# Optimization experiments

Hardware: AMD Instinct MI355X
Metric: run time of the kernel (lower is better)

Reference implementation:

```python
import jax, jax.numpy as jnp
import numpy as np

D_MODEL = 1024
NUM_HEADS = 16
HEAD_DIM = D_MODEL // NUM_HEADS


def setup_inputs() -> dict:
    key = jax.random.key(0)
    ks = jax.random.split(key, 11)
    B, N = 2, 2048
    s = 1.0 / np.sqrt(D_MODEL)
    return {
        "query": jax.random.normal(ks[0], (B, N, D_MODEL), jnp.float32),
        "key":   jax.random.normal(ks[1], (B, N, D_MODEL), jnp.float32),
        "value": jax.random.normal(ks[2], (B, N, D_MODEL), jnp.float32),
        "Wq": jax.random.normal(ks[3], (D_MODEL, D_MODEL), jnp.float32) * s,
        "bq": jax.random.normal(ks[4], (D_MODEL,), jnp.float32) * 0.01,
        "Wk": jax.random.normal(ks[5], (D_MODEL, D_MODEL), jnp.float32) * s,
        "bk": jax.random.normal(ks[6], (D_MODEL,), jnp.float32) * 0.01,
        "Wv": jax.random.normal(ks[7], (D_MODEL, D_MODEL), jnp.float32) * s,
        "bv": jax.random.normal(ks[8], (D_MODEL,), jnp.float32) * 0.01,
        "Wo": jax.random.normal(ks[9], (D_MODEL, D_MODEL), jnp.float32) * s,
        "bo": jax.random.normal(ks[10], (D_MODEL,), jnp.float32) * 0.01,
    }


def _split_heads(x):
    # [B, N, d_model] -> [B, H, N, head_dim]
    B, N, _ = x.shape
    return x.reshape(B, N, NUM_HEADS, HEAD_DIM).transpose(0, 2, 1, 3)


def reference(query, key, value, Wq, bq, Wk, bk, Wv, bv, Wo, bo):
    B, N, _ = query.shape
    q = _split_heads(query @ Wq.T + bq)  # [B,H,N,dh]
    k = _split_heads(key @ Wk.T + bk)
    v = _split_heads(value @ Wv.T + bv)
    # NOTE: faithful to source: no 1/sqrt(head_dim) scaling.
    scores = jnp.einsum("bhnd,bhmd->bhnm", q, k)
    attn = jax.nn.softmax(scores, axis=-1)
    out = jnp.einsum("bhnm,bhmd->bhnd", attn, v)
    out = out.transpose(0, 2, 1, 3).reshape(B, N, D_MODEL)
    return out @ Wo.T + bo
```

## Files before the change

### kernel.cpp

```cpp
#include <hip/hip_runtime.h>
#include <cstdint>

#define DEV __device__ __forceinline__

typedef __bf16 bf16x8 __attribute__((ext_vector_type(8)));
typedef short s16x8 __attribute__((ext_vector_type(8)));
typedef float f32x4 __attribute__((ext_vector_type(4)));
typedef unsigned short u16;

constexpr int D_MODEL = 1024;
constexpr int SEQ = 2048;
constexpr float LOG2E = 1.4426950408889634f;
constexpr float SHIFT = 64.0f;

DEV u16 f2bf(float f) {
  uint32_t u = __float_as_uint(f);
  u += 0x7fff + ((u >> 16) & 1);
  return (u16)(u >> 16);
}

DEV void load_lds16(const void* g, void* l) {
  __builtin_amdgcn_global_load_lds((const __attribute__((address_space(1))) void*)g,
                                   (__attribute__((address_space(3))) void*)l, 16, 0, 0);
}

struct ConvArgs {
  const float* src[7];
  u16* dst[7];
};

__global__ __launch_bounds__(256) void convert_kernel(ConvArgs a) {
  const int bid = blockIdx.x;
  int t, base;
  if (bid < 12288) { t = bid >> 12; base = (bid & 4095) << 10; }
  else { int r = bid - 12288; t = 3 + (r >> 10); base = (r & 1023) << 10; }
  const int i = base + threadIdx.x * 4;
  const float4 v = *(const float4*)(a.src[t] + i);
  ushort4 o;
  o.x = f2bf(v.x); o.y = f2bf(v.y); o.z = f2bf(v.z); o.w = f2bf(v.w);
  *(ushort4*)(a.dst[t] + i) = o;
}

struct GemmArgs {
  const u16* A[3];
  const u16* W[3];
  const float* bias[3];
  u16* out[3];
  float scale[3];
};

__global__ __launch_bounds__(256, 2) void gemm_qkv(GemmArgs args) {
  __shared__ u16 lds[2][2][128 * 64];
  const int bid = blockIdx.x;
  const int xcd = bid & 7, j = bid >> 3;
  const int z = j >> 5;
  const int r0 = j & 31;
  const int m0 = (xcd * 4 + (r0 >> 3)) * 128;
  const int n0 = (r0 & 7) * 128;
  const u16* __restrict__ A = args.A[z];
  const u16* __restrict__ W = args.W[z];
  const int tid = threadIdx.x;
  const int lane = tid & 63, wid = tid >> 6;
  const int quad = lane >> 4, l16 = lane & 15;
  const int wm = wid >> 1, wn = wid & 1;

  f32x4 acc[4][4] = {};

#define GSTAGE(T, B)                                                              \
  {                                                                               \
    _Pragma("unroll")                                                             \
    for (int p = 0; p < 4; ++p) {                                                 \
      int c = p * 256 + tid;                                                      \
      int row = c >> 3;                                                           \
      int g = ((c & 7) ^ (row & 7)) * 8;                                          \
      load_lds16(A + (size_t)(m0 + row) * D_MODEL + (T) * 64 + g, &lds[B][0][c * 8]); \
      load_lds16(W + (size_t)(n0 + row) * D_MODEL + (T) * 64 + g, &lds[B][1][c * 8]); \
    }                                                                             \
  }

  GSTAGE(0, 0);
  __syncthreads();

  for (int kt = 0; kt < 16; ++kt) {
    if (kt + 1 < 16) GSTAGE(kt + 1, (kt + 1) & 1);
    const u16* lA = lds[kt & 1][0];
    const u16* lB = lds[kt & 1][1];
#pragma unroll
    for (int ks = 0; ks < 2; ++ks) {
      bf16x8 af[4], bfr[4];
#pragma unroll
      for (int mt = 0; mt < 4; ++mt) {
        int r = wm * 64 + mt * 16 + l16;
        int ch = (ks * 4 + quad) ^ (r & 7);
        af[mt] = *(const bf16x8*)&lA[r * 64 + ch * 8];
      }
#pragma unroll
      for (int nt = 0; nt < 4; ++nt) {
        int r = wn * 64 + nt * 16 + l16;
        int ch = (ks * 4 + quad) ^ (r & 7);
        bfr[nt] = *(const bf16x8*)&lB[r * 64 + ch * 8];
      }
#pragma unroll
      for (int mt = 0; mt < 4; ++mt)
#pragma unroll
        for (int nt = 0; nt < 4; ++nt)
          acc[mt][nt] = __builtin_amdgcn_mfma_f32_16x16x32_bf16(af[mt], bfr[nt], acc[mt][nt], 0, 0, 0);
    }
    __syncthreads();
  }
#undef GSTAGE

  const float* __restrict__ bias = args.bias[z];
  u16* out = args.out[z];
  float sc = args.scale[z];
  if (z == 2) {
#pragma unroll
    for (int nt = 0; nt < 4; ++nt) {
      int col = n0 + wn * 64 + nt * 16 + l16;
      float bv = bias[col];
      int h = col >> 6, d = col & 63;
#pragma unroll
      for (int mt = 0; mt < 4; ++mt) {
        int mb = m0 + wm * 64 + mt * 16 + quad * 4;
        int b = mb >> 11, tt = mb & 2047;
        ushort4 o;
        o.x = f2bf(acc[mt][nt][0] + bv);
        o.y = f2bf(acc[mt][nt][1] + bv);
        o.z = f2bf(acc[mt][nt][2] + bv);
        o.w = f2bf(acc[mt][nt][3] + bv);
        *(ushort4*)(out + ((size_t)(b * 16 + h) * 64 + d) * SEQ + tt) = o;
      }
    }
  } else {
#pragma unroll
    for (int nt = 0; nt < 4; ++nt) {
      int col = n0 + wn * 64 + nt * 16 + l16;
      float bv = bias[col];
      int h = col >> 6, d = col & 63;
#pragma unroll
      for (int mt = 0; mt < 4; ++mt) {
        int mb = m0 + wm * 64 + mt * 16 + quad * 4;
#pragma unroll
        for (int r = 0; r < 4; ++r) {
          int tok = mb + r;
          int b = tok >> 11, tt = tok & 2047;
          out[(((size_t)(b * 16 + h) * SEQ + tt) << 6) + d] = f2bf((acc[mt][nt][r] + bv) * sc);
        }
      }
    }
  }
}

__global__ __launch_bounds__(256, 2) void gemm_out(const u16* __restrict__ A,
                                                   const u16* __restrict__ W,
                                                   const float* __restrict__ bias,
                                                   float* __restrict__ out) {
  __shared__ u16 lds[2][(128 + 64) * 64];
  const int bid = blockIdx.x;
  const int xcd = bid & 7, j = bid >> 3;
  const int m0 = (xcd * 4 + (j >> 4)) * 128;
  const int n0 = (j & 15) * 64;
  const int tid = threadIdx.x;
  const int lane = tid & 63, wid = tid >> 6;
  const int quad = lane >> 4, l16 = lane & 15;
  const int wm = wid >> 1, wn = wid & 1;

  f32x4 acc[4][2] = {};

#define OSTAGE(T, B)                                                              \
  {                                                                               \
    _Pragma("unroll")                                                             \
    for (int p = 0; p < 4; ++p) {                                                 \
      int c = p * 256 + tid;                                                      \
      int row = c >> 3;                                                           \
      int g = ((c & 7) ^ (row & 7)) * 8;                                          \
      load_lds16(A + (size_t)(m0 + row) * D_MODEL + (T) * 64 + g, &lds[B][c * 8]); \
    }                                                                             \
    _Pragma("unroll")                                                             \
    for (int p = 0; p < 2; ++p) {                                                 \
      int c = p * 256 + tid;                                                      \
      int row = c >> 3;                                                           \
      int g = ((c & 7) ^ (row & 7)) * 8;                                          \
      load_lds16(W + (size_t)(n0 + row) * D_MODEL + (T) * 64 + g,                 \
                 &lds[B][128 * 64 + c * 8]);                                      \
    }                                                                             \
  }

  OSTAGE(0, 0);
  __syncthreads();

  for (int kt = 0; kt < 16; ++kt) {
    if (kt + 1 < 16) OSTAGE(kt + 1, (kt + 1) & 1);
    const u16* lA = lds[kt & 1];
    const u16* lW = lds[kt & 1] + 128 * 64;
#pragma unroll
    for (int ks = 0; ks < 2; ++ks) {
      bf16x8 af[4], wf[2];
#pragma unroll
      for (int mt = 0; mt < 4; ++mt) {
        int r = wm * 64 + mt * 16 + l16;
        int ch = (ks * 4 + quad) ^ (r & 7);
        af[mt] = *(const bf16x8*)&lA[r * 64 + ch * 8];
      }
#pragma unroll
      for (int nt = 0; nt < 2; ++nt) {
        int r = wn * 32 + nt * 16 + l16;
        int ch = (ks * 4 + quad) ^ (r & 7);
        wf[nt] = *(const bf16x8*)&lW[r * 64 + ch * 8];
      }
#pragma unroll
      for (int mt = 0; mt < 4; ++mt)
#pragma unroll
        for (int nt = 0; nt < 2; ++nt)
          acc[mt][nt] = __builtin_amdgcn_mfma_f32_16x16x32_bf16(af[mt], wf[nt], acc[mt][nt], 0, 0, 0);
    }
    __syncthreads();
  }
#undef OSTAGE

#pragma unroll
  for (int nt = 0; nt < 2; ++nt) {
    int col = n0 + wn * 32 + nt * 16 + l16;
    float bv = bias[col];
#pragma unroll
    for (int mt = 0; mt < 4; ++mt) {
      int mb = m0 + wm * 64 + mt * 16 + quad * 4;
#pragma unroll
      for (int r = 0; r < 4; ++r)
        out[(size_t)(mb + r) * D_MODEL + col] = acc[mt][nt][r] + bv;
    }
  }
}

__global__ __launch_bounds__(512, 4) void attn_kernel(const u16* __restrict__ Q,
                                                      const u16* __restrict__ K,
                                                      const u16* __restrict__ Vt,
                                                      u16* __restrict__ O) {
  __shared__ u16 sm[4][2][64 * 64];
  const int bid = blockIdx.x;
  const int xcd = bid & 7, jj = bid >> 3;
  const int bh = xcd + 8 * (jj >> 4);
  const int q0 = (jj & 15) * 128;
  const int tid = threadIdx.x;
  const int lane = tid & 63, w = tid >> 6;
  const int quad = lane >> 4, l16 = lane & 15;
  const int kb = w & 1;
  const int pair = w >> 1;

  const u16* kbase = K + (size_t)bh * SEQ * 64;
  const u16* vtbase = Vt + (size_t)bh * 64 * SEQ;

  bf16x8 qf[2][2];
#pragma unroll
  for (int qh = 0; qh < 2; ++qh) {
    const u16* qrow = Q + ((size_t)bh * SEQ + q0 + pair * 32 + qh * 16 + l16) * 64;
    qf[qh][0] = *(const bf16x8*)(qrow + quad * 8);
    qf[qh][1] = *(const bf16x8*)(qrow + 32 + quad * 8);
  }

  bf16x8 onesA;
  {
    __bf16 v = (l16 == 0) ? (__bf16)1.0f : (__bf16)0.0f;
#pragma unroll
    for (int j = 0; j < 8; ++j) onesA[j] = v;
  }

  f32x4 acc[2][5] = {};
  const f32x4 minit = {-SHIFT, -SHIFT, -SHIFT, -SHIFT};

#define STAGE(T, B)                                                               \
  {                                                                               \
    int c = tid;                                                                  \
    int row = c >> 3;                                                             \
    int km = (row & 32) | (((row >> 2) & 3) << 3) | (((row >> 4) & 1) << 2) |     \
             (row & 3);                                                           \
    int g = ((c & 7) ^ (row & 7)) * 8;                                            \
    load_lds16(kbase + (size_t)((T) * 64 + km) * 64 + g, &sm[B][0][c * 8]);       \
    load_lds16(vtbase + (size_t)row * SEQ + (T) * 64 + g, &sm[B][1][c * 8]);      \
  }

  STAGE(0, 0);
  STAGE(1, 1);
  STAGE(2, 2);
  asm volatile("s_waitcnt vmcnt(4)" ::: "memory");
  __builtin_amdgcn_s_barrier();
  __builtin_amdgcn_sched_barrier(0);

  for (int t = 0; t < SEQ / 64; ++t) {
    if (t + 3 < SEQ / 64) STAGE(t + 3, (t + 3) & 3);
    const u16* lK = sm[t & 3][0];
    const u16* lV = sm[t & 3][1];

    bf16x8 kf[2][2];
#pragma unroll
    for (int nt = 0; nt < 2; ++nt) {
      int r = kb * 32 + nt * 16 + l16;
#pragma unroll
      for (int ks = 0; ks < 2; ++ks) {
        int ch = (ks * 4 + quad) ^ (r & 7);
        kf[nt][ks] = *(const bf16x8*)&lK[r * 64 + ch * 8];
      }
    }

    f32x4 s[2][2];
    __builtin_amdgcn_s_setprio(1);
#pragma unroll
    for (int qh = 0; qh < 2; ++qh) {
      s[qh][0] = __builtin_amdgcn_mfma_f32_16x16x32_bf16(kf[0][0], qf[qh][0], minit, 0, 0, 0);
      s[qh][0] = __builtin_amdgcn_mfma_f32_16x16x32_bf16(kf[0][1], qf[qh][1], s[qh][0], 0, 0, 0);
      s[qh][1] = __builtin_amdgcn_mfma_f32_16x16x32_bf16(kf[1][0], qf[qh][0], minit, 0, 0, 0);
      s[qh][1] = __builtin_amdgcn_mfma_f32_16x16x32_bf16(kf[1][1], qf[qh][1], s[qh][1], 0, 0, 0);
    }
    __builtin_amdgcn_s_setprio(0);

    s16x8 pf[2];
#pragma unroll
    for (int qh = 0; qh < 2; ++qh) {
      bf16x8 pb;
#pragma unroll
      for (int r = 0; r < 4; ++r) {
        pb[r] = (__bf16)__builtin_amdgcn_exp2f(s[qh][0][r]);
        pb[4 + r] = (__bf16)__builtin_amdgcn_exp2f(s[qh][1][r]);
      }
      pf[qh] = __builtin_bit_cast(s16x8, pb);
    }

    bf16x8 vf[4];
#pragma unroll
    for (int dt = 0; dt < 4; ++dt) {
      int row = dt * 16 + l16;
      int ch = (kb * 4 + quad) ^ (row & 7);
      vf[dt] = *(const bf16x8*)&lV[row * 64 + ch * 8];
    }
    __builtin_amdgcn_s_setprio(1);
#pragma unroll
    for (int dt = 0; dt < 4; ++dt)
#pragma unroll
      for (int qh = 0; qh < 2; ++qh)
        acc[qh][dt] = __builtin_amdgcn_mfma_f32_16x16x32_bf16(
            vf[dt], __builtin_bit_cast(bf16x8, pf[qh]), acc[qh][dt], 0, 0, 0);
#pragma unroll
    for (int qh = 0; qh < 2; ++qh)
      acc[qh][4] = __builtin_amdgcn_mfma_f32_16x16x32_bf16(
          onesA, __builtin_bit_cast(bf16x8, pf[qh]), acc[qh][4], 0, 0, 0);
    __builtin_amdgcn_s_setprio(0);

    if (t <= SEQ / 64 - 4) {
      asm volatile("s_waitcnt vmcnt(4)" ::: "memory");
      __builtin_amdgcn_s_barrier();
      __builtin_amdgcn_sched_barrier(0);
    } else if (t == SEQ / 64 - 3) {
      asm volatile("s_waitcnt vmcnt(2)" ::: "memory");
      __builtin_amdgcn_s_barrier();
      __builtin_amdgcn_sched_barrier(0);
    } else if (t == SEQ / 64 - 2) {
      asm volatile("s_waitcnt vmcnt(0)" ::: "memory");
      __builtin_amdgcn_s_barrier();
      __builtin_amdgcn_sched_barrier(0);
    }
  }
#undef STAGE

  __syncthreads();

  float* red = (float*)&sm[0][0][0];
  if (kb == 1) {
#pragma unroll
    for (int qh = 0; qh < 2; ++qh)
#pragma unroll
      for (int dt = 0; dt < 5; ++dt)
        *(f32x4*)&red[(((pair * 2 + qh) * 5 + dt) * 64 + lane) * 4] = acc[qh][dt];
  }
  __syncthreads();
  if (kb == 0) {
    const int b = bh >> 4, h = bh & 15;
#pragma unroll
    for (int qh = 0; qh < 2; ++qh) {
#pragma unroll
      for (int dt = 0; dt < 5; ++dt)
        acc[qh][dt] += *(const f32x4*)&red[(((pair * 2 + qh) * 5 + dt) * 64 + lane) * 4];
      float sum = __shfl(acc[qh][4][0], l16, 64);
      float inv = 1.0f / sum;
      const int tok = b * SEQ + q0 + pair * 32 + qh * 16 + l16;
      u16* obase = O + (size_t)tok * D_MODEL + h * 64;
#pragma unroll
      for (int dt = 0; dt < 4; ++dt) {
        ushort4 o;
        o.x = f2bf(acc[qh][dt][0] * inv);
        o.y = f2bf(acc[qh][dt][1] * inv);
        o.z = f2bf(acc[qh][dt][2] * inv);
        o.w = f2bf(acc[qh][dt][3] * inv);
        *(ushort4*)(obase + dt * 16 + quad * 4) = o;
      }
    }
  }
}

extern "C" void kernel_launch(void* const* d_in, const int* in_sizes, int n_in,
                              void* d_out, int out_size, void* d_ws, size_t ws_size,
                              hipStream_t stream) {
  const float* q  = (const float*)d_in[0];
  const float* k  = (const float*)d_in[1];
  const float* v  = (const float*)d_in[2];
  const float* Wq = (const float*)d_in[3];
  const float* bq = (const float*)d_in[4];
  const float* Wk = (const float*)d_in[5];
  const float* bk = (const float*)d_in[6];
  const float* Wv = (const float*)d_in[7];
  const float* bv = (const float*)d_in[8];
  const float* Wo = (const float*)d_in[9];
  const float* bo = (const float*)d_in[10];

  uint8_t* ws = (uint8_t*)d_ws;
  const size_t MB = 1024 * 1024;
  u16* Xq  = (u16*)(ws + 0 * MB);
  u16* Xk  = (u16*)(ws + 8 * MB);
  u16* Xv  = (u16*)(ws + 16 * MB);
  u16* Wqb = (u16*)(ws + 24 * MB);
  u16* Wkb = (u16*)(ws + 26 * MB);
  u16* Wvb = (u16*)(ws + 28 * MB);
  u16* Wob = (u16*)(ws + 30 * MB);
  u16* Qb  = (u16*)(ws + 32 * MB);
  u16* Kb  = (u16*)(ws + 40 * MB);
  u16* Vtb = (u16*)(ws + 48 * MB);
  u16* Ob  = Xq;

  ConvArgs ca;
  ca.src[0] = q;  ca.dst[0] = Xq;
  ca.src[1] = k;  ca.dst[1] = Xk;
  ca.src[2] = v;  ca.dst[2] = Xv;
  ca.src[3] = Wq; ca.dst[3] = Wqb;
  ca.src[4] = Wk; ca.dst[4] = Wkb;
  ca.src[5] = Wv; ca.dst[5] = Wvb;
  ca.src[6] = Wo; ca.dst[6] = Wob;
  convert_kernel<<<dim3(16384), 256, 0, stream>>>(ca);

  GemmArgs ga;
  ga.A[0] = Xq; ga.A[1] = Xk; ga.A[2] = Xv;
  ga.W[0] = Wqb; ga.W[1] = Wkb; ga.W[2] = Wvb;
  ga.bias[0] = bq; ga.bias[1] = bk; ga.bias[2] = bv;
  ga.out[0] = Qb; ga.out[1] = Kb; ga.out[2] = Vtb;
  ga.scale[0] = LOG2E; ga.scale[1] = 1.0f; ga.scale[2] = 1.0f;
  gemm_qkv<<<dim3(768), 256, 0, stream>>>(ga);

  attn_kernel<<<dim3(512), 512, 0, stream>>>(Qb, Kb, Vtb, Ob);

  gemm_out<<<dim3(512), 256, 0, stream>>>(Ob, Wob, bo, (float*)d_out);
}
```

Baseline: 204.8 us.

## Load K/V MFMA fragments directly from global into registers, dropping LDS staging

Replaces the 4-stage LDS ring buffer (global_load_lds plus per-tile barriers) with per-wave direct global loads of K and V^T fragments into registers. Each fragment is prefetched one tile ahead. This removes LDS traffic and block-wide barriers, and shrinks shared memory to just the reduction buffer. In exchange, each of the 4 wave pairs redundantly fetches the same K/V tiles from global/L2, and only one tile of latency hiding remains.

```diff
diff --git a/kernel.cpp b/kernel.cpp
--- a/kernel.cpp
+++ b/kernel.cpp
@@ -236,7 +236,7 @@
                                                       const u16* __restrict__ K,
                                                       const u16* __restrict__ Vt,
                                                       u16* __restrict__ O) {
-  __shared__ u16 sm[4][2][64 * 64];
+  __shared__ float red[8 * 5 * 64 * 4];
   const int bid = blockIdx.x;
   const int xcd = bid & 7, jj = bid >> 3;
   const int bh = xcd + 8 * (jj >> 4);
@@ -268,40 +268,21 @@
   f32x4 acc[2][5] = {};
   const f32x4 minit = {-SHIFT, -SHIFT, -SHIFT, -SHIFT};
 
-#define STAGE(T, B)                                                               \
-  {                                                                               \
-    int c = tid;                                                                  \
-    int row = c >> 3;                                                             \
-    int km = (row & 32) | (((row >> 2) & 3) << 3) | (((row >> 4) & 1) << 2) |     \
-             (row & 3);                                                           \
-    int g = ((c & 7) ^ (row & 7)) * 8;                                            \
-    load_lds16(kbase + (size_t)((T) * 64 + km) * 64 + g, &sm[B][0][c * 8]);       \
-    load_lds16(vtbase + (size_t)row * SEQ + (T) * 64 + g, &sm[B][1][c * 8]);      \
-  }
-
-  STAGE(0, 0);
-  STAGE(1, 1);
-  STAGE(2, 2);
-  asm volatile("s_waitcnt vmcnt(4)" ::: "memory");
-  __builtin_amdgcn_s_barrier();
-  __builtin_amdgcn_sched_barrier(0);
+  const int kmbase = kb * 32 + (l16 >> 2) * 8 + (l16 & 3);
+  const u16* kp = kbase + (size_t)kmbase * 64 + quad * 8;
+  const u16* vp = vtbase + (size_t)l16 * SEQ + kb * 32 + quad * 8;
+
+  bf16x8 kf[2][2], vf[4];
+  kf[0][0] = *(const bf16x8*)(kp);
+  kf[0][1] = *(const bf16x8*)(kp + 32);
+  kf[1][0] = *(const bf16x8*)(kp + 256);
+  kf[1][1] = *(const bf16x8*)(kp + 288);
+  vf[0] = *(const bf16x8*)(vp);
+  vf[1] = *(const bf16x8*)(vp + 16 * SEQ);
+  vf[2] = *(const bf16x8*)(vp + 32 * SEQ);
+  vf[3] = *(const bf16x8*)(vp + 48 * SEQ);
 
   for (int t = 0; t < SEQ / 64; ++t) {
-    if (t + 3 < SEQ / 64) STAGE(t + 3, (t + 3) & 3);
-    const u16* lK = sm[t & 3][0];
-    const u16* lV = sm[t & 3][1];
-
-    bf16x8 kf[2][2];
-#pragma unroll
-    for (int nt = 0; nt < 2; ++nt) {
-      int r = kb * 32 + nt * 16 + l16;
-#pragma unroll
-      for (int ks = 0; ks < 2; ++ks) {
-        int ch = (ks * 4 + quad) ^ (r & 7);
-        kf[nt][ks] = *(const bf16x8*)&lK[r * 64 + ch * 8];
-      }
-    }
-
     f32x4 s[2][2];
     __builtin_amdgcn_s_setprio(1);
 #pragma unroll
@@ -313,6 +294,14 @@
     }
     __builtin_amdgcn_s_setprio(0);
 
+    if (t + 1 < SEQ / 64) {
+      kp += 64 * 64;
+      kf[0][0] = *(const bf16x8*)(kp);
+      kf[0][1] = *(const bf16x8*)(kp + 32);
+      kf[1][0] = *(const bf16x8*)(kp + 256);
+      kf[1][1] = *(const bf16x8*)(kp + 288);
+    }
+
     s16x8 pf[2];
 #pragma unroll
     for (int qh = 0; qh < 2; ++qh) {
@@ -325,13 +314,6 @@
       pf[qh] = __builtin_bit_cast(s16x8, pb);
     }
 
-    bf16x8 vf[4];
-#pragma unroll
-    for (int dt = 0; dt < 4; ++dt) {
-      int row = dt * 16 + l16;
-      int ch = (kb * 4 + quad) ^ (row & 7);
-      vf[dt] = *(const bf16x8*)&lV[row * 64 + ch * 8];
-    }
     __builtin_amdgcn_s_setprio(1);
 #pragma unroll
     for (int dt = 0; dt < 4; ++dt)
@@ -345,25 +327,15 @@
           onesA, __builtin_bit_cast(bf16x8, pf[qh]), acc[qh][4], 0, 0, 0);
     __builtin_amdgcn_s_setprio(0);
 
-    if (t <= SEQ / 64 - 4) {
-      asm volatile("s_waitcnt vmcnt(4)" ::: "memory");
-      __builtin_amdgcn_s_barrier();
-      __builtin_amdgcn_sched_barrier(0);
-    } else if (t == SEQ / 64 - 3) {
-      asm volatile("s_waitcnt vmcnt(2)" ::: "memory");
-      __builtin_amdgcn_s_barrier();
-      __builtin_amdgcn_sched_barrier(0);
-    } else if (t == SEQ / 64 - 2) {
-      asm volatile("s_waitcnt vmcnt(0)" ::: "memory");
-      __builtin_amdgcn_s_barrier();
-      __builtin_amdgcn_sched_barrier(0);
-    }
-  }
-#undef STAGE
-
-  __syncthreads();
-
-  float* red = (float*)&sm[0][0][0];
+    if (t + 1 < SEQ / 64) {
+      vp += 64;
+      vf[0] = *(const bf16x8*)(vp);
+      vf[1] = *(const bf16x8*)(vp + 16 * SEQ);
+      vf[2] = *(const bf16x8*)(vp + 32 * SEQ);
+      vf[3] = *(const bf16x8*)(vp + 48 * SEQ);
+    }
+  }
+
   if (kb == 1) {
 #pragma unroll
     for (int qh = 0; qh < 2; ++qh)
```

After: 276.1 us. 1.35x slower.

## Software-pipeline QK^T one tile ahead of exp and PV in attention loop

Applied to the files above, without the earlier changes.

Computes the QK^T scores for tile t+1 before the exp/PV work of tile t, so score MFMAs overlap with the exponentials and value reads, and tightens the vmcnt waits so the next tile's data is resident one iteration earlier. It also lowers the launch-bounds occupancy hint from 4 to 2 blocks per CU to free registers for the extra live score fragments. The cost is fewer resident waves for latency hiding, shallower effective prefetch slack, and more register pressure.

```diff
diff --git a/kernel.cpp b/kernel.cpp
--- a/kernel.cpp
+++ b/kernel.cpp
@@ -232,7 +232,7 @@
   }
 }
 
-__global__ __launch_bounds__(512, 4) void attn_kernel(const u16* __restrict__ Q,
+__global__ __launch_bounds__(512, 2) void attn_kernel(const u16* __restrict__ Q,
                                                       const u16* __restrict__ K,
                                                       const u16* __restrict__ Vt,
                                                       u16* __restrict__ O) {
@@ -279,39 +279,46 @@
     load_lds16(vtbase + (size_t)row * SEQ + (T) * 64 + g, &sm[B][1][c * 8]);      \
   }
 
+#define SCLUSTER(T, dst)                                                          \
+  {                                                                               \
+    const u16* lK = sm[(T) & 3][0];                                               \
+    bf16x8 kf[2][2];                                                              \
+    _Pragma("unroll")                                                             \
+    for (int nt = 0; nt < 2; ++nt) {                                              \
+      int r = kb * 32 + nt * 16 + l16;                                            \
+      _Pragma("unroll")                                                           \
+      for (int ks = 0; ks < 2; ++ks) {                                            \
+        int ch = (ks * 4 + quad) ^ (r & 7);                                       \
+        kf[nt][ks] = *(const bf16x8*)&lK[r * 64 + ch * 8];                        \
+      }                                                                           \
+    }                                                                             \
+    __builtin_amdgcn_s_setprio(1);                                                \
+    _Pragma("unroll")                                                             \
+    for (int qh = 0; qh < 2; ++qh) {                                              \
+      dst[qh][0] = __builtin_amdgcn_mfma_f32_16x16x32_bf16(kf[0][0], qf[qh][0], minit, 0, 0, 0); \
+      dst[qh][0] = __builtin_amdgcn_mfma_f32_16x16x32_bf16(kf[0][1], qf[qh][1], dst[qh][0], 0, 0, 0); \
+      dst[qh][1] = __builtin_amdgcn_mfma_f32_16x16x32_bf16(kf[1][0], qf[qh][0], minit, 0, 0, 0); \
+      dst[qh][1] = __builtin_amdgcn_mfma_f32_16x16x32_bf16(kf[1][1], qf[qh][1], dst[qh][1], 0, 0, 0); \
+    }                                                                             \
+    __builtin_amdgcn_s_setprio(0);                                                \
+  }
+
   STAGE(0, 0);
   STAGE(1, 1);
   STAGE(2, 2);
-  asm volatile("s_waitcnt vmcnt(4)" ::: "memory");
+  asm volatile("s_waitcnt vmcnt(2)" ::: "memory");
   __builtin_amdgcn_s_barrier();
   __builtin_amdgcn_sched_barrier(0);
 
+  f32x4 sP[2][2];
+  SCLUSTER(0, sP);
+
+#pragma unroll 2
   for (int t = 0; t < SEQ / 64; ++t) {
     if (t + 3 < SEQ / 64) STAGE(t + 3, (t + 3) & 3);
-    const u16* lK = sm[t & 3][0];
-    const u16* lV = sm[t & 3][1];
-
-    bf16x8 kf[2][2];
-#pragma unroll
-    for (int nt = 0; nt < 2; ++nt) {
-      int r = kb * 32 + nt * 16 + l16;
-#pragma unroll
-      for (int ks = 0; ks < 2; ++ks) {
-        int ch = (ks * 4 + quad) ^ (r & 7);
-        kf[nt][ks] = *(const bf16x8*)&lK[r * 64 + ch * 8];
-      }
-    }
-
-    f32x4 s[2][2];
-    __builtin_amdgcn_s_setprio(1);
-#pragma unroll
-    for (int qh = 0; qh < 2; ++qh) {
-      s[qh][0] = __builtin_amdgcn_mfma_f32_16x16x32_bf16(kf[0][0], qf[qh][0], minit, 0, 0, 0);
-      s[qh][0] = __builtin_amdgcn_mfma_f32_16x16x32_bf16(kf[0][1], qf[qh][1], s[qh][0], 0, 0, 0);
-      s[qh][1] = __builtin_amdgcn_mfma_f32_16x16x32_bf16(kf[1][0], qf[qh][0], minit, 0, 0, 0);
-      s[qh][1] = __builtin_amdgcn_mfma_f32_16x16x32_bf16(kf[1][1], qf[qh][1], s[qh][1], 0, 0, 0);
-    }
-    __builtin_amdgcn_s_setprio(0);
+
+    f32x4 sN[2][2];
+    if (t + 1 < SEQ / 64) SCLUSTER(t + 1, sN);
 
     s16x8 pf[2];
 #pragma unroll
@@ -319,12 +326,13 @@
       bf16x8 pb;
 #pragma unroll
       for (int r = 0; r < 4; ++r) {
-        pb[r] = (__bf16)__builtin_amdgcn_exp2f(s[qh][0][r]);
-        pb[4 + r] = (__bf16)__builtin_amdgcn_exp2f(s[qh][1][r]);
+        pb[r] = (__bf16)__builtin_amdgcn_exp2f(sP[qh][0][r]);
+        pb[4 + r] = (__bf16)__builtin_amdgcn_exp2f(sP[qh][1][r]);
       }
       pf[qh] = __builtin_bit_cast(s16x8, pb);
     }
 
+    const u16* lV = sm[t & 3][1];
     bf16x8 vf[4];
 #pragma unroll
     for (int dt = 0; dt < 4; ++dt) {
@@ -345,21 +353,26 @@
           onesA, __builtin_bit_cast(bf16x8, pf[qh]), acc[qh][4], 0, 0, 0);
     __builtin_amdgcn_s_setprio(0);
 
-    if (t <= SEQ / 64 - 4) {
-      asm volatile("s_waitcnt vmcnt(4)" ::: "memory");
+    if (t + 1 < SEQ / 64) {
+#pragma unroll
+      for (int qh = 0; qh < 2; ++qh) {
+        sP[qh][0] = sN[qh][0];
+        sP[qh][1] = sN[qh][1];
+      }
+    }
+
+    if (t < SEQ / 64 - 3) {
+      asm volatile("s_waitcnt vmcnt(2)" ::: "memory");
       __builtin_amdgcn_s_barrier();
       __builtin_amdgcn_sched_barrier(0);
     } else if (t == SEQ / 64 - 3) {
-      asm volatile("s_waitcnt vmcnt(2)" ::: "memory");
-      __builtin_amdgcn_s_barrier();
-      __builtin_amdgcn_sched_barrier(0);
-    } else if (t == SEQ / 64 - 2) {
       asm volatile("s_waitcnt vmcnt(0)" ::: "memory");
       __builtin_amdgcn_s_barrier();
       __builtin_amdgcn_sched_barrier(0);
     }
   }
 #undef STAGE
+#undef SCLUSTER
 
   __syncthreads();
 
```

After: 211.5 us. 3.3% more time.

## Triple-buffer QKV GEMM with K-tile 32, manual vmcnt waits and setprio

Applied to the files above, without the earlier changes.

Rewrites the QKV projection GEMM main loop to use three LDS stages with a K-tile of 32 instead of two stages of 64. Partial vmcnt waits keep two tiles of global-to-LDS loads in flight across barriers, s_setprio is raised around the MFMA block, and the smaller LDS footprint allows launch bounds of 3 blocks per CU. The swizzle is adapted to the 4-chunk row layout. The trade-off is twice as many barriers per K and a hand-tuned waitcnt that must match the load count.

```diff
diff --git a/kernel.cpp b/kernel.cpp
--- a/kernel.cpp
+++ b/kernel.cpp
@@ -49,8 +49,8 @@
   float scale[3];
 };
 
-__global__ __launch_bounds__(256, 2) void gemm_qkv(GemmArgs args) {
-  __shared__ u16 lds[2][2][128 * 64];
+__global__ __launch_bounds__(256, 3) void gemm_qkv(GemmArgs args) {
+  __shared__ u16 lds[3][2][128 * 32];
   const int bid = blockIdx.x;
   const int xcd = bid & 7, j = bid >> 3;
   const int z = j >> 5;
@@ -69,44 +69,55 @@
 #define GSTAGE(T, B)                                                              \
   {                                                                               \
     _Pragma("unroll")                                                             \
-    for (int p = 0; p < 4; ++p) {                                                 \
+    for (int p = 0; p < 2; ++p) {                                                 \
       int c = p * 256 + tid;                                                      \
-      int row = c >> 3;                                                           \
-      int g = ((c & 7) ^ (row & 7)) * 8;                                          \
-      load_lds16(A + (size_t)(m0 + row) * D_MODEL + (T) * 64 + g, &lds[B][0][c * 8]); \
-      load_lds16(W + (size_t)(n0 + row) * D_MODEL + (T) * 64 + g, &lds[B][1][c * 8]); \
+      int row = c >> 2;                                                           \
+      int g = ((c & 3) ^ ((row >> 1) & 3)) * 8;                                   \
+      load_lds16(A + (size_t)(m0 + row) * D_MODEL + (T) * 32 + g, &lds[B][0][c * 8]); \
+      load_lds16(W + (size_t)(n0 + row) * D_MODEL + (T) * 32 + g, &lds[B][1][c * 8]); \
     }                                                                             \
   }
 
   GSTAGE(0, 0);
-  __syncthreads();
-
-  for (int kt = 0; kt < 16; ++kt) {
-    if (kt + 1 < 16) GSTAGE(kt + 1, (kt + 1) & 1);
-    const u16* lA = lds[kt & 1][0];
-    const u16* lB = lds[kt & 1][1];
-#pragma unroll
-    for (int ks = 0; ks < 2; ++ks) {
-      bf16x8 af[4], bfr[4];
-#pragma unroll
-      for (int mt = 0; mt < 4; ++mt) {
-        int r = wm * 64 + mt * 16 + l16;
-        int ch = (ks * 4 + quad) ^ (r & 7);
-        af[mt] = *(const bf16x8*)&lA[r * 64 + ch * 8];
-      }
-#pragma unroll
-      for (int nt = 0; nt < 4; ++nt) {
-        int r = wn * 64 + nt * 16 + l16;
-        int ch = (ks * 4 + quad) ^ (r & 7);
-        bfr[nt] = *(const bf16x8*)&lB[r * 64 + ch * 8];
-      }
-#pragma unroll
-      for (int mt = 0; mt < 4; ++mt)
-#pragma unroll
-        for (int nt = 0; nt < 4; ++nt)
-          acc[mt][nt] = __builtin_amdgcn_mfma_f32_16x16x32_bf16(af[mt], bfr[nt], acc[mt][nt], 0, 0, 0);
-    }
-    __syncthreads();
+  GSTAGE(1, 1);
+  asm volatile("s_waitcnt vmcnt(4)" ::: "memory");
+  __builtin_amdgcn_s_barrier();
+  __builtin_amdgcn_sched_barrier(0);
+
+  for (int kt = 0; kt < 32; ++kt) {
+    if (kt + 2 < 32) GSTAGE(kt + 2, (kt + 2) % 3);
+    const u16* lA = lds[kt % 3][0];
+    const u16* lB = lds[kt % 3][1];
+    bf16x8 af[4], bfr[4];
+#pragma unroll
+    for (int mt = 0; mt < 4; ++mt) {
+      int r = wm * 64 + mt * 16 + l16;
+      int ch = quad ^ ((r >> 1) & 3);
+      af[mt] = *(const bf16x8*)&lA[r * 32 + ch * 8];
+    }
+#pragma unroll
+    for (int nt = 0; nt < 4; ++nt) {
+      int r = wn * 64 + nt * 16 + l16;
+      int ch = quad ^ ((r >> 1) & 3);
+      bfr[nt] = *(const bf16x8*)&lB[r * 32 + ch * 8];
+    }
+    __builtin_amdgcn_s_setprio(1);
+#pragma unroll
+    for (int mt = 0; mt < 4; ++mt)
+#pragma unroll
+      for (int nt = 0; nt < 4; ++nt)
+        acc[mt][nt] = __builtin_amdgcn_mfma_f32_16x16x32_bf16(af[mt], bfr[nt], acc[mt][nt], 0, 0, 0);
+    __builtin_amdgcn_s_setprio(0);
+
+    if (kt < 30) {
+      asm volatile("s_waitcnt vmcnt(4)" ::: "memory");
+      __builtin_amdgcn_s_barrier();
+      __builtin_amdgcn_sched_barrier(0);
+    } else if (kt == 30) {
+      asm volatile("s_waitcnt vmcnt(0)" ::: "memory");
+      __builtin_amdgcn_s_barrier();
+      __builtin_amdgcn_sched_barrier(0);
+    }
   }
 #undef GSTAGE
 
```

Result: faster. 199.6 us, median of 2 (-2.5%).
